# Kernel tuning notes

Measured on AMD Instinct MI355X. Metric: run time of the kernel, lower is better.

The kernel has to match this reference:

```python
import jax, jax.numpy as jnp
import numpy as np

T, L, M = 3, 4, 3            # tasks, layers, modules-per-layer
B, C, H, W = 8, 64, 128, 128 # input NCHW
OUT_C = 3                    # decoder output channels
TAU = 1.0                    # gumbel temperature (set_tau equivalent)
TASKS = ["semantic", "depth", "normal"]


def setup_inputs() -> dict:
    key = jax.random.key(0)
    ks = jax.random.split(key, 8)
    x = jax.random.normal(ks[0], (B, C, H, W), jnp.float32)
    # architecture parameters: layer0 [T,1,M], layers 1..L-1 [T,M,M] (const_v=0.001)
    alpha0 = 0.001 * jax.random.normal(ks[1], (T, 1, M), jnp.float32)
    alphas = 0.001 * jax.random.normal(ks[2], (L - 1, T, M, M), jnp.float32)
    # gumbels: -log(Exp(1)) == standard Gumbel == -log(-log(U))
    u0 = jax.random.uniform(ks[3], (T, 1, M), jnp.float32, 1e-6, 1.0)
    g0 = -jnp.log(-jnp.log(u0))
    u = jax.random.uniform(ks[4], (L - 1, T, M, M), jnp.float32, 1e-6, 1.0)
    gs = -jnp.log(-jnp.log(u))
    # encoder conv banks: [L, M, C, C, 3, 3] (OIHW per module), He-ish init
    enc_w = (1.0 / np.sqrt(C * 9)) * jax.random.normal(ks[5], (L, M, C, C, 3, 3), jnp.float32)
    enc_b = jnp.zeros((L, M, C), jnp.float32)
    # per-task 1x1 conv decoders
    dec_w = (1.0 / np.sqrt(C)) * jax.random.normal(ks[6], (T, OUT_C, C, 1, 1), jnp.float32)
    dec_b = jnp.zeros((T, OUT_C), jnp.float32)
    return dict(x=x, alpha0=alpha0, alphas=alphas, g0=g0, gs=gs,
                enc_w=enc_w, enc_b=enc_b, dec_w=dec_w, dec_b=dec_b)


def _conv(x, w, b):
    y = jax.lax.conv_general_dilated(x, w, (1, 1), 'SAME',
                                     dimension_numbers=('NCHW', 'OIHW', 'NCHW'))
    return y + b[None, :, None, None]


def _task_forward(x, t, alpha0, alphas, g0, gs, enc_w, enc_b):
    """Sequential gumbel top-1 straight-through routing + selected-encoder apply."""
    h = x
    idx = jnp.int32(0)  # input_ID
    for layer in range(L):
        if layer == 0:
            a = alpha0[t, 0]           # [M]
            g = g0[t, 0]
        else:
            a = alphas[layer - 1, t][idx]   # dynamic gather on previous index
            g = gs[layer - 1, t][idx]
        logits = (jax.nn.log_softmax(a) + g) / TAU
        probs = jax.nn.softmax(logits)
        new_idx = jnp.argmax(probs).astype(jnp.int32)
        # straight-through scale: 1 in fwd, grad flows through probs[new_idx]
        p_sel = probs[new_idx]
        st_scale = 1.0 - jax.lax.stop_gradient(p_sel) + p_sel
        w = enc_w[layer][new_idx]  # gather only the selected module's weights
        b = enc_b[layer][new_idx]
        h = jax.nn.relu(_conv(h * st_scale, w, b))
        idx = new_idx
    return h


def _forward(x, alpha0, alphas, g0, gs, enc_w, enc_b, dec_w, dec_b):
    outs = []
    for t, t_name in enumerate(TASKS):
        h = _task_forward(x, t, alpha0, alphas, g0, gs, enc_w, enc_b)
        y = _conv(h, dec_w[t], dec_b[t])  # decoder (1x1 conv)
        # F.interpolate to (im_h, im_w) is identity here (spatial size preserved)
        if 'normal' in t_name:
            y = y / jnp.linalg.norm(y, axis=1, keepdims=True)
        outs.append(y)
    return jnp.stack(outs)  # [T, B, OUT_C, H, W]


def reference(x, alpha0, alphas, g0, gs, enc_w, enc_b, dec_w, dec_b):
    return _forward(x, alpha0, alphas, g0, gs, enc_w, enc_b, dec_w, dec_b)
```

## Files before the change

### kernel.cpp

```cpp
#include <hip/hip_runtime.h>

#define BB 8
#define CC 64
#define HH 128
#define WW 128
#define TT 3
#define LL 4
#define MM 3

#define PW 130
#define CHP ((size_t)PW * PW * 16)
#define IMGH ((size_t)PW * PW * CC)

typedef _Float16 half8 __attribute__((ext_vector_type(8)));
typedef _Float16 half4 __attribute__((ext_vector_type(4)));
typedef float floatx16 __attribute__((ext_vector_type(16)));

__device__ __forceinline__ void async_ld16(const _Float16* g, _Float16* l) {
    __builtin_amdgcn_global_load_lds(
        (const __attribute__((address_space(1))) void*)g,
        (__attribute__((address_space(3))) void*)l, 16, 0, 0);
}

__global__ __launch_bounds__(256) void prep_weights(
    const float* __restrict__ enc_w,
    const float* __restrict__ alpha0,
    const float* __restrict__ alphas,
    const float* __restrict__ g0,
    const float* __restrict__ gs,
    int* __restrict__ sel,
    _Float16* __restrict__ W3)
{
    int tl = blockIdx.y;
    int t = tl >> 2, layer = tl & 3;
    int idx = 0;
    for (int l = 0; l <= layer; ++l) {
        const float *a, *g;
        if (l == 0) { a = alpha0 + t * MM; g = g0 + t * MM; }
        else {
            int off = (((l - 1) * TT + t) * MM + idx) * MM;
            a = alphas + off; g = gs + off;
        }
        float best = a[0] + g[0];
        int bi = 0;
        for (int j = 1; j < MM; ++j) {
            float v = a[j] + g[j];
            if (v > best) { best = v; bi = j; }
        }
        idx = bi;
    }
    const int m = idx;
    if (blockIdx.x == 0 && threadIdx.x == 0) sel[tl] = m;

    const float* src = enc_w + ((size_t)layer * MM + m) * (CC * CC * 9);
    _Float16* dst = W3 + (size_t)tl * 36864;
    for (int i = blockIdx.x * 256 + threadIdx.x; i < 36864; i += gridDim.x * 256) {
        int j   = i & 7;
        int l   = (i >> 3) & 63;
        int o   = (i >> 9) & 1;
        int il  = (i >> 10) & 1;
        int c   = (i >> 11) & 1;
        int tap = i >> 12;
        int oc  = o * 32 + (l & 31);
        int kch = c * 32 + il * 16 + (l >> 5) * 8 + j;
        dst[i] = (_Float16)src[(oc * CC + kch) * 9 + tap];
    }
}

__global__ __launch_bounds__(256) void zero_borders(_Float16* __restrict__ base0)
{
    _Float16* base = base0 + (size_t)blockIdx.x * IMGH;
    const int i0 = blockIdx.y * 1032;
    for (int i = i0 + threadIdx.x; i < i0 + 1032; i += 256) {
        int pl  = i / 1032;
        int rem = i - pl * 1032;
        int px_idx = rem >> 1, sh = rem & 1;
        int row, col;
        if (px_idx < 130)      { row = 0;            col = px_idx; }
        else if (px_idx < 260) { row = 129;          col = px_idx - 130; }
        else if (px_idx < 388) { row = px_idx - 259; col = 0; }
        else                   { row = px_idx - 387; col = 129; }
        half8 z = {};
        *(half8*)(base + (size_t)pl * CHP + ((size_t)row * PW + col) * 16 + sh * 8) = z;
    }
}

__global__ __launch_bounds__(256) void to_chunked(
    const float* __restrict__ x,
    _Float16* __restrict__ act0)
{
    const int xs = blockIdx.x;
    const int y  = blockIdx.y;
    const int b  = blockIdx.z;

    __shared__ _Float16 lds[64 * 72];

    const int wv = threadIdx.x >> 6;
    const int l  = threadIdx.x & 63;
    const float* src = x + ((size_t)b * CC * HH + y) * WW + xs * 64 + l;
#pragma unroll
    for (int k = 0; k < 16; ++k) {
        int ch = wv * 16 + k;
        lds[l * 72 + ch] = (_Float16)src[(size_t)ch * HH * WW];
    }
    __syncthreads();
    int px = threadIdx.x & 63;
    int q  = threadIdx.x >> 6;
    _Float16* dst = act0 + (size_t)b * IMGH + (size_t)q * CHP
                  + ((size_t)(y + 1) * PW + xs * 64 + px + 1) * 16;
    *(half8*)dst       = *(const half8*)&lds[px * 72 + q * 16];
    *(half8*)(dst + 8) = *(const half8*)&lds[px * 72 + q * 16 + 8];
}

__global__ __launch_bounds__(256, 2) void conv3x3_mfma(
    const _Float16* __restrict__ in,
    _Float16* __restrict__ out,
    const _Float16* __restrict__ W3,
    const float* __restrict__ enc_b,
    const int* __restrict__ sel,
    int layer, int task0, size_t tsi, size_t tso)
{
    const int nwg  = gridDim.x * gridDim.y * gridDim.z;
    const int flat = blockIdx.x + gridDim.x * (blockIdx.y + gridDim.y * blockIdx.z);
    const int q8   = nwg >> 3;
    const int logical = (flat & 7) * q8 + (flat >> 3);
    const int bx  = logical & 31;
    const int rem = logical >> 5;
    const int b   = rem & 7;
    const int tz  = rem >> 3;

    const int y0  = (bx >> 1) * 8;
    const int px0 = (bx & 1) * 64;
    const int t   = task0 + tz;

    const _Float16* inp = in + (size_t)tz * tsi + (size_t)b * IMGH;
    _Float16* outp      = out + (size_t)tz * tso + (size_t)b * IMGH;
    const int tl = t * LL + layer;
    const _Float16* Wt = W3 + (size_t)tl * 36864;

    const int tid  = threadIdx.x;
    const int lane = tid & 63;
    const int w    = tid >> 6;
    const int n    = lane & 31;
    const int ksub = lane >> 5;

    __shared__ __align__(16) _Float16 lds[2 * 10752 + 2 * 9216];
    _Float16* actb0 = lds;
    _Float16* actb1 = lds + 10752;
    _Float16* wtb0  = lds + 21504;
    _Float16* wtb1  = lds + 21504 + 9216;

    floatx16 acc[2][2][2];
#pragma unroll
    for (int rr = 0; rr < 2; ++rr)
#pragma unroll
        for (int o = 0; o < 2; ++o)
#pragma unroll
            for (int j = 0; j < 2; ++j)
#pragma unroll
                for (int i = 0; i < 16; ++i) acc[rr][o][j][i] = 0.f;

    int preoff[3][2];
#pragma unroll
    for (int dx = 0; dx < 3; ++dx)
#pragma unroll
        for (int h = 0; h < 2; ++h) {
            int pxv = dx + n + 32 * h;
            preoff[dx][h] = pxv * 16 + ((ksub ^ ((pxv >> 2) & 1)) << 3);
        }

#define STAGE(p, actd, wtd)                                                    \
    {                                                                          \
        const _Float16* plane = inp + (size_t)(p) * CHP;                       \
        for (int j = w; j < 21; j += 4) {                                      \
            int si = j * 64 + lane;                      \
            int s16 = si & 1;                                                  \
            int u = si >> 1;                                      \
            if (u > 659) u = 659;                    \
            int r = (u * 993) >> 16;                \
            int px = u - r * 66;                                               \
            const _Float16* src =                                              \
                plane + ((size_t)(y0 + r) * PW + (px0 + px)) * 16              \
                      + ((s16 ^ ((px >> 2) & 1)) << 3);                        \
            async_ld16(src, (actd) + j * 512);                                 \
        }                                                                      \
        const int c_ = (p) >> 1, il_ = (p) & 1;                                \
        for (int k = w; k < 18; k += 4) {                                      \
            const _Float16* src =                                              \
                Wt + ((k >> 1) * 8 + c_ * 4 + il_ * 2 + (k & 1)) * 512         \
                   + lane * 8;                                                 \
            async_ld16(src, (wtd) + k * 512);                                  \
        }                                                                      \
    }

#define COMPUTE(al, wl)                                                        \
    {                                                                          \
        __builtin_amdgcn_s_setprio(1);                                         \
        _Pragma("unroll")                                                      \
        for (int tap = 0; tap < 9; ++tap) {                                    \
            const int dy = tap / 3;                                            \
            const int dx = tap - dy * 3;                                       \
            half8 a0 = *(const half8*)((wl) + (tap * 2 + 0) * 512 + lane * 8); \
            half8 a1 = *(const half8*)((wl) + (tap * 2 + 1) * 512 + lane * 8); \
            _Pragma("unroll")                                                  \
            for (int rr = 0; rr < 2; ++rr) {                                   \
                const _Float16* lb = (al) + (2 * w + rr + dy) * 1056;          \
                half8 b0 = *(const half8*)(lb + preoff[dx][0]);                \
                half8 b1 = *(const half8*)(lb + preoff[dx][1]);                \
                acc[rr][0][0] = __builtin_amdgcn_mfma_f32_32x32x16_f16(a0, b0, acc[rr][0][0], 0, 0, 0); \
                acc[rr][0][1] = __builtin_amdgcn_mfma_f32_32x32x16_f16(a0, b1, acc[rr][0][1], 0, 0, 0); \
                acc[rr][1][0] = __builtin_amdgcn_mfma_f32_32x32x16_f16(a1, b0, acc[rr][1][0], 0, 0, 0); \
                acc[rr][1][1] = __builtin_amdgcn_mfma_f32_32x32x16_f16(a1, b1, acc[rr][1][1], 0, 0, 0); \
            }                                                                  \
        }                                                                      \
        __builtin_amdgcn_s_setprio(0);                                         \
    }

    STAGE(0, actb0, wtb0);
    __syncthreads();

    STAGE(1, actb1, wtb1);
    __builtin_amdgcn_sched_barrier(0);
    COMPUTE(actb0, wtb0);
    __syncthreads();

    STAGE(2, actb0, wtb0);
    __builtin_amdgcn_sched_barrier(0);
    COMPUTE(actb1, wtb1);
    __syncthreads();

    STAGE(3, actb1, wtb1);
    __builtin_amdgcn_sched_barrier(0);
    COMPUTE(actb0, wtb0);
    __syncthreads();

    COMPUTE(actb1, wtb1);
#undef STAGE
#undef COMPUTE

    int m = sel[t * LL + layer];
    m = __builtin_amdgcn_readfirstlane(m);
    const float* Bp = enc_b + ((size_t)layer * MM + m) * CC;
#pragma unroll
    for (int rr = 0; rr < 2; ++rr) {
#pragma unroll
        for (int o = 0; o < 2; ++o)
#pragma unroll
            for (int j = 0; j < 2; ++j) {
                int px = px0 + j * 32 + n;
                size_t pxi = (size_t)(y0 + 2 * w + rr + 1) * PW + px + 1;
#pragma unroll
                for (int rg = 0; rg < 4; ++rg) {
                    int oci = 4 * ksub + 8 * rg;
                    int pl  = o * 2 + (oci >> 4);
                    _Float16* po = outp + (size_t)pl * CHP + pxi * 16 + (oci & 15);
                    half4 h;
#pragma unroll
                    for (int k = 0; k < 4; ++k)
                        h[k] = (_Float16)fmaxf(acc[rr][o][j][rg * 4 + k]
                                               + Bp[o * 32 + oci + k], 0.f);
                    *(half4*)po = h;
                }
            }
    }
}

__global__ __launch_bounds__(256) void decoder_kernel(
    const _Float16* __restrict__ in,
    size_t ts,
    const float* __restrict__ dec_w,
    const float* __restrict__ dec_b,
    float* __restrict__ out,
    int task0, int ntask)
{
    const int HW = HH * WW;
    int gid = blockIdx.x * 256 + threadIdx.x;
    if (gid >= ntask * BB * HW) return;
    int tz = gid / (BB * HW);
    int rem = gid - tz * (BB * HW);
    int b = rem / HW;
    int px = rem - b * HW;
    int t = task0 + tz;
    int y = px >> 7;
    int xx = px & 127;

    const _Float16* base = in + (size_t)tz * ts + (size_t)b * IMGH;
    size_t pxi = ((size_t)(y + 1) * PW + xx + 1) * 16;
    const float* w = dec_w + (size_t)t * 3 * CC;

    float a0 = dec_b[t * 3 + 0];
    float a1 = dec_b[t * 3 + 1];
    float a2 = dec_b[t * 3 + 2];
#pragma unroll
    for (int il = 0; il < 4; ++il) {
        const _Float16* hp = base + (size_t)il * CHP + pxi;
#pragma unroll
        for (int cc = 0; cc < 16; cc += 8) {
            half8 h = *(const half8*)(hp + cc);
#pragma unroll
            for (int k = 0; k < 8; ++k) {
                float v = (float)h[k];
                int ch = il * 16 + cc + k;
                a0 += v * w[ch];
                a1 += v * w[CC + ch];
                a2 += v * w[2 * CC + ch];
            }
        }
    }
    if (t == 2) {
        float r = 1.0f / sqrtf(a0 * a0 + a1 * a1 + a2 * a2);
        a0 *= r; a1 *= r; a2 *= r;
    }
    float* ob = out + ((size_t)t * BB + b) * 3 * HW + px;
    ob[0]      = a0;
    ob[HW]     = a1;
    ob[2 * HW] = a2;
}

extern "C" void kernel_launch(void* const* d_in, const int* in_sizes, int n_in,
                              void* d_out, int out_size, void* d_ws, size_t ws_size,
                              hipStream_t stream) {
    const float* x      = (const float*)d_in[0];
    const float* alpha0 = (const float*)d_in[1];
    const float* alphas = (const float*)d_in[2];
    const float* g0     = (const float*)d_in[3];
    const float* gs     = (const float*)d_in[4];
    const float* enc_w  = (const float*)d_in[5];
    const float* enc_b  = (const float*)d_in[6];
    const float* dec_w  = (const float*)d_in[7];
    const float* dec_b  = (const float*)d_in[8];
    float* out = (float*)d_out;

    const size_t ACT = (size_t)BB * IMGH;
    char* pw = (char*)d_ws;
    int* sel = (int*)pw;                 pw += 1024;
    _Float16* W3 = (_Float16*)pw;        pw += (size_t)12 * 36864 * 2;
    _Float16* act0 = (_Float16*)pw;      pw += ACT * 2;
    _Float16* bufs = (_Float16*)pw;
    size_t base = (size_t)(pw - (char*)d_ws);
    bool fused = ws_size >= base + 6 * ACT * 2;

    prep_weights<<<dim3(36, 12), 256, 0, stream>>>(enc_w, alpha0, alphas, g0, gs, sel, W3);
    int nbuf = fused ? 7 : 3;
    zero_borders<<<dim3(nbuf * BB, 4), 256, 0, stream>>>(act0);
    to_chunked<<<dim3(2, HH, BB), 256, 0, stream>>>(x, act0);

    if (fused) {
        _Float16* A = bufs;
        _Float16* B = bufs + ACT;
        size_t ts = 2 * ACT;
        conv3x3_mfma<<<dim3(32, BB, 3), 256, 0, stream>>>(act0, A, W3, enc_b, sel, 0, 0, 0,  ts);
        conv3x3_mfma<<<dim3(32, BB, 3), 256, 0, stream>>>(A,    B, W3, enc_b, sel, 1, 0, ts, ts);
        conv3x3_mfma<<<dim3(32, BB, 3), 256, 0, stream>>>(B,    A, W3, enc_b, sel, 2, 0, ts, ts);
        conv3x3_mfma<<<dim3(32, BB, 3), 256, 0, stream>>>(A,    B, W3, enc_b, sel, 3, 0, ts, ts);
        decoder_kernel<<<(3 * BB * HH * WW + 255) / 256, 256, 0, stream>>>(
            B, ts, dec_w, dec_b, out, 0, 3);
    } else {
        _Float16* A = bufs;
        _Float16* B = bufs + ACT;
        for (int t = 0; t < TT; ++t) {
            conv3x3_mfma<<<dim3(32, BB, 1), 256, 0, stream>>>(act0, A, W3, enc_b, sel, 0, t, 0, 0);
            conv3x3_mfma<<<dim3(32, BB, 1), 256, 0, stream>>>(A,    B, W3, enc_b, sel, 1, t, 0, 0);
            conv3x3_mfma<<<dim3(32, BB, 1), 256, 0, stream>>>(B,    A, W3, enc_b, sel, 2, t, 0, 0);
            conv3x3_mfma<<<dim3(32, BB, 1), 256, 0, stream>>>(A,    B, W3, enc_b, sel, 3, t, 0, 0);
            decoder_kernel<<<(BB * HH * WW + 255) / 256, 256, 0, stream>>>(
                B, 0, dec_w, dec_b, out, t, 1);
        }
    }
}
```

Measured before the change: 241.2 us.

## Use explicit vmcnt waits for double-buffered conv staging and drop fused-task launch path

Each wave now issues exactly ten unrolled async LDS loads per stage, covering both activations and weights. A partial `s_waitcnt vmcnt(10)` plus raw `s_barrier` replaces `__syncthreads`, so the next stage's global loads stay in flight while the current buffer is computed. The host side drops the workspace-dependent fused path that processed all three tasks in one grid. It now always runs a per-task loop of four conv launches and one decoder launch. This lowers workspace needs but triples launch count and shrinks each grid, which can cost occupancy and launch overhead.

```diff
diff --git a/kernel.cpp b/kernel.cpp
--- a/kernel.cpp
+++ b/kernel.cpp
@@ -172,24 +172,28 @@
 #define STAGE(p, actd, wtd)                                                    \
     {                                                                          \
         const _Float16* plane = inp + (size_t)(p) * CHP;                       \
-        for (int j = w; j < 21; j += 4) {                                      \
-            int si = j * 64 + lane;                      \
-            int s16 = si & 1;                                                  \
-            int u = si >> 1;                                      \
-            if (u > 659) u = 659;                    \
-            int r = (u * 993) >> 16;                \
-            int px = u - r * 66;                                               \
-            const _Float16* src =                                              \
-                plane + ((size_t)(y0 + r) * PW + (px0 + px)) * 16              \
-                      + ((s16 ^ ((px >> 2) & 1)) << 3);                        \
-            async_ld16(src, (actd) + j * 512);                                 \
-        }                                                                      \
         const int c_ = (p) >> 1, il_ = (p) & 1;                                \
-        for (int k = w; k < 18; k += 4) {                                      \
-            const _Float16* src =                                              \
-                Wt + ((k >> 1) * 8 + c_ * 4 + il_ * 2 + (k & 1)) * 512         \
-                   + lane * 8;                                                 \
-            async_ld16(src, (wtd) + k * 512);                                  \
+        _Pragma("unroll")                                                      \
+        for (int k10 = 0; k10 < 10; ++k10) {                                   \
+            int q = w + 4 * k10;                             \
+            if (q < 21) {                                                      \
+                int si = q * 64 + lane;                  \
+                int s16 = si & 1;                                              \
+                int u = si >> 1;                                  \
+                if (u > 659) u = 659;                  \
+                int r = (u * 993) >> 16;            \
+                int px = u - r * 66;                                           \
+                const _Float16* src =                                          \
+                    plane + ((size_t)(y0 + r) * PW + (px0 + px)) * 16          \
+                          + ((s16 ^ ((px >> 2) & 1)) << 3);                    \
+                async_ld16(src, (actd) + q * 512);                             \
+            } else {                                                           \
+                int k = q - 21; if (k > 17) k = 17;        \
+                const _Float16* src =                                          \
+                    Wt + ((k >> 1) * 8 + c_ * 4 + il_ * 2 + (k & 1)) * 512     \
+                       + lane * 8;                                             \
+                async_ld16(src, (wtd) + k * 512);                              \
+            }                                                                  \
         }                                                                      \
     }
 
@@ -216,27 +220,32 @@
         __builtin_amdgcn_s_setprio(0);                                         \
     }
 
+#define WAITN(nlit)                                                            \
+    asm volatile("s_waitcnt vmcnt(" #nlit ")" ::: "memory");                   \
+    __builtin_amdgcn_sched_barrier(0)
+#define BAR()                                                                  \
+    __builtin_amdgcn_sched_barrier(0);                                         \
+    __builtin_amdgcn_s_barrier();                                              \
+    __builtin_amdgcn_sched_barrier(0)
+
     STAGE(0, actb0, wtb0);
-    __syncthreads();
-
     STAGE(1, actb1, wtb1);
-    __builtin_amdgcn_sched_barrier(0);
+    WAITN(10); BAR();
     COMPUTE(actb0, wtb0);
-    __syncthreads();
-
+    BAR();
     STAGE(2, actb0, wtb0);
-    __builtin_amdgcn_sched_barrier(0);
+    WAITN(10); BAR();
     COMPUTE(actb1, wtb1);
-    __syncthreads();
-
+    BAR();
     STAGE(3, actb1, wtb1);
-    __builtin_amdgcn_sched_barrier(0);
+    WAITN(10); BAR();
     COMPUTE(actb0, wtb0);
-    __syncthreads();
-
+    WAITN(0); BAR();
     COMPUTE(actb1, wtb1);
 #undef STAGE
 #undef COMPUTE
+#undef WAITN
+#undef BAR
 
     int m = sel[t * LL + layer];
     m = __builtin_amdgcn_readfirstlane(m);
@@ -336,35 +345,19 @@
     int* sel = (int*)pw;                 pw += 1024;
     _Float16* W3 = (_Float16*)pw;        pw += (size_t)12 * 36864 * 2;
     _Float16* act0 = (_Float16*)pw;      pw += ACT * 2;
-    _Float16* bufs = (_Float16*)pw;
-    size_t base = (size_t)(pw - (char*)d_ws);
-    bool fused = ws_size >= base + 6 * ACT * 2;
+    _Float16* A = (_Float16*)pw;         pw += ACT * 2;
+    _Float16* B = (_Float16*)pw;
 
     prep_weights<<<dim3(36, 12), 256, 0, stream>>>(enc_w, alpha0, alphas, g0, gs, sel, W3);
-    int nbuf = fused ? 7 : 3;
-    zero_borders<<<dim3(nbuf * BB, 4), 256, 0, stream>>>(act0);
+    zero_borders<<<dim3(3 * BB, 4), 256, 0, stream>>>(act0);
     to_chunked<<<dim3(2, HH, BB), 256, 0, stream>>>(x, act0);
 
-    if (fused) {
-        _Float16* A = bufs;
-        _Float16* B = bufs + ACT;
-        size_t ts = 2 * ACT;
-        conv3x3_mfma<<<dim3(32, BB, 3), 256, 0, stream>>>(act0, A, W3, enc_b, sel, 0, 0, 0,  ts);
-        conv3x3_mfma<<<dim3(32, BB, 3), 256, 0, stream>>>(A,    B, W3, enc_b, sel, 1, 0, ts, ts);
-        conv3x3_mfma<<<dim3(32, BB, 3), 256, 0, stream>>>(B,    A, W3, enc_b, sel, 2, 0, ts, ts);
-        conv3x3_mfma<<<dim3(32, BB, 3), 256, 0, stream>>>(A,    B, W3, enc_b, sel, 3, 0, ts, ts);
-        decoder_kernel<<<(3 * BB * HH * WW + 255) / 256, 256, 0, stream>>>(
-            B, ts, dec_w, dec_b, out, 0, 3);
-    } else {
-        _Float16* A = bufs;
-        _Float16* B = bufs + ACT;
-        for (int t = 0; t < TT; ++t) {
-            conv3x3_mfma<<<dim3(32, BB, 1), 256, 0, stream>>>(act0, A, W3, enc_b, sel, 0, t, 0, 0);
-            conv3x3_mfma<<<dim3(32, BB, 1), 256, 0, stream>>>(A,    B, W3, enc_b, sel, 1, t, 0, 0);
-            conv3x3_mfma<<<dim3(32, BB, 1), 256, 0, stream>>>(B,    A, W3, enc_b, sel, 2, t, 0, 0);
-            conv3x3_mfma<<<dim3(32, BB, 1), 256, 0, stream>>>(A,    B, W3, enc_b, sel, 3, t, 0, 0);
-            decoder_kernel<<<(BB * HH * WW + 255) / 256, 256, 0, stream>>>(
-                B, 0, dec_w, dec_b, out, t, 1);
-        }
-    }
-}
+    for (int t = 0; t < TT; ++t) {
+        conv3x3_mfma<<<dim3(32, BB, 1), 256, 0, stream>>>(act0, A, W3, enc_b, sel, 0, t, 0, 0);
+        conv3x3_mfma<<<dim3(32, BB, 1), 256, 0, stream>>>(A,    B, W3, enc_b, sel, 1, t, 0, 0);
+        conv3x3_mfma<<<dim3(32, BB, 1), 256, 0, stream>>>(B,    A, W3, enc_b, sel, 2, t, 0, 0);
+        conv3x3_mfma<<<dim3(32, BB, 1), 256, 0, stream>>>(A,    B, W3, enc_b, sel, 3, t, 0, 0);
+        decoder_kernel<<<(BB * HH * WW + 255) / 256, 256, 0, stream>>>(
+            B, 0, dec_w, dec_b, out, t, 1);
+    }
+}
```

Measured after the change: 288.4 us. 1.2x slower.
